# Performance work log

Measured on AMD Instinct MI355X. Metric: run time of the kernel, lower is better.

## Reference

```python
import jax, jax.numpy as jnp
from jax import lax
import numpy as np

D = 1024      # input_size
H = D // 2    # proj hidden
T = 25        # num_ner_labels
B, S = 64, 512


def setup_inputs() -> dict:
    key = jax.random.key(0)
    ks = jax.random.split(key, 8)
    sc1 = 1.0 / np.sqrt(D)
    sc2 = 1.0 / np.sqrt(H)
    return {
        "encoder_out": jax.random.normal(ks[0], (B, S, D), dtype=jnp.float32),
        "W1": jax.random.uniform(ks[1], (D, H), jnp.float32, -sc1, sc1),
        "b1": jax.random.uniform(ks[2], (H,), jnp.float32, -sc1, sc1),
        "W2": jax.random.uniform(ks[3], (H, T), jnp.float32, -sc2, sc2),
        "b2": jax.random.uniform(ks[4], (T,), jnp.float32, -sc2, sc2),
        "start_trans": jax.random.uniform(ks[5], (T,), jnp.float32, -0.1, 0.1),
        "end_trans": jax.random.uniform(ks[6], (T,), jnp.float32, -0.1, 0.1),
        "trans": jax.random.uniform(ks[7], (T, T), jnp.float32, -0.1, 0.1),
        "ner_labels": jax.random.randint(jax.random.fold_in(key, 1), (B, S), 0, T, dtype=jnp.int64),
        "mask": jnp.ones((B, S), dtype=bool),
    }


def _crf_nll(emissions, start_trans, end_trans, trans, labels, mask):
    # torchcrf negative mean log-likelihood, batch_first
    maskf = mask.astype(emissions.dtype)
    # numerator: score of gold path
    em_at_tag = jnp.take_along_axis(emissions, labels[..., None], axis=2)[..., 0]  # [B,S]
    score0 = start_trans[labels[:, 0]] + em_at_tag[:, 0]
    trans_sc = trans[labels[:, :-1], labels[:, 1:]]                                # [B,S-1]
    step_score = (trans_sc + em_at_tag[:, 1:]) * maskf[:, 1:]
    last_idx = mask.sum(axis=1).astype(jnp.int32) - 1
    last_tag = jnp.take_along_axis(labels, last_idx[:, None].astype(labels.dtype), axis=1)[:, 0]
    numerator = score0 + step_score.sum(axis=1) + end_trans[last_tag]
    # denominator: log partition via forward algorithm (scan over time)
    alpha0 = start_trans[None, :] + emissions[:, 0]                                # [B,T]
    em_rest = jnp.swapaxes(emissions[:, 1:], 0, 1)                                 # [S-1,B,T]
    m_rest = jnp.swapaxes(mask[:, 1:], 0, 1)                                       # [S-1,B]

    def step(alpha, xs):
        em_t, m_t = xs
        new = jax.scipy.special.logsumexp(
            alpha[:, :, None] + trans[None, :, :] + em_t[:, None, :], axis=1)
        return jnp.where(m_t[:, None], new, alpha), None

    alpha, _ = lax.scan(step, alpha0, (em_rest, m_rest))
    log_Z = jax.scipy.special.logsumexp(alpha + end_trans[None, :], axis=1)        # [B]
    return -jnp.mean(numerator - log_Z)


def reference(encoder_out, W1, b1, W2, b2, start_trans, end_trans, trans, ner_labels, mask):
    h = jax.nn.gelu(encoder_out @ W1 + b1, approximate=False)  # dropout is eval-mode identity
    emissions = h @ W2 + b2                                    # [B,S,T]
    return _crf_nll(emissions, start_trans, end_trans, trans, ner_labels, mask)
```

## Files before the change

kernel.cpp:

```cpp
#include <hip/hip_runtime.h>
#include <math.h>

#define DD 1024
#define HH 512
#define TT 25
#define BB 64
#define SS 512
#define MM (BB*SS)
#define NC 32

typedef __attribute__((ext_vector_type(8))) short short8;
typedef __attribute__((ext_vector_type(4))) float floatx4;
typedef __attribute__((ext_vector_type(16))) float floatx16;

static __device__ __forceinline__ unsigned short f2bf(float f) {
  unsigned u = __float_as_uint(f);
  u = (u + 0x7FFFu + ((u >> 16) & 1u)) >> 16;
  return (unsigned short)u;
}
static __device__ __forceinline__ float bf2f(unsigned short s) {
  return __uint_as_float(((unsigned)s) << 16);
}
static __device__ __forceinline__ float rl(float v, int i) {
  return __int_as_float(__builtin_amdgcn_readlane(__float_as_int(v), i));
}
static __device__ __forceinline__ void load_lds16(const void* g, void* l) {
  __builtin_amdgcn_global_load_lds(
      (const __attribute__((address_space(1))) unsigned int*)g,
      (__attribute__((address_space(3))) unsigned int*)l, 16, 0, 0);
}
union U4S8 { uint4 u; short8 s; };

__global__ __launch_bounds__(256) void k_prep(
    const float* __restrict__ W1, const float* __restrict__ W2,
    unsigned short* __restrict__ W1T2, unsigned short* __restrict__ W2p) {
  const int t = threadIdx.x;
  if (blockIdx.y < 8) {
    __shared__ unsigned short tile[64 * 72];
    const int k0 = blockIdx.x * 64, n0 = blockIdx.y * 64;
    #pragma unroll
    for (int it = 0; it < 16; it++) {
      int idx = t + it * 256;
      int kk = idx >> 6, nn = idx & 63;
      tile[nn * 72 + kk] = f2bf(W1[(size_t)(k0 + kk) * HH + n0 + nn]);
    }
    __syncthreads();
    #pragma unroll
    for (int it = 0; it < 4; it++) {
      int idx = (t + it * 256) * 4;
      int nn = idx >> 6, kk = idx & 63;
      ushort4 v;
      v.x = tile[nn * 72 + kk];     v.y = tile[nn * 72 + kk + 1];
      v.z = tile[nn * 72 + kk + 2]; v.w = tile[nn * 72 + kk + 3];
      int kt = (k0 >> 5) + (kk >> 5), kkk = kk & 31;
      *(ushort4*)(W1T2 + (size_t)kt * (HH * 32) + (n0 + nn) * 32 + kkk) = v;
    }
  } else {
    #pragma unroll
    for (int e = 0; e < 4; e++) {
      int idx = blockIdx.x * 1024 + t + e * 256;
      int row = idx >> 9, k = idx & 511;
      float v = (row < TT) ? W2[(size_t)k * TT + row] : 0.f;
      W2p[(size_t)row * HH + k] = f2bf(v);
    }
  }
}

__global__ __launch_bounds__(256, 3) void k_emis(
    const float* __restrict__ X, const unsigned short* __restrict__ W1T2,
    const float* __restrict__ b1, const unsigned short* __restrict__ W2p,
    const float* __restrict__ b2, float* __restrict__ em) {
  __shared__ __attribute__((aligned(16))) short lds[20480];

  const int tid  = threadIdx.x;
  const int lane = tid & 63;
  const int w    = tid >> 6;
  const int l15  = lane & 15;
  const int kc   = lane >> 4;
  const int m0   = blockIdx.x * 64;
  const int colbase = blockIdx.y * 256;

  floatx4 acc[4][4];
  #pragma unroll
  for (int a = 0; a < 4; a++)
    #pragma unroll
    for (int b = 0; b < 4; b++)
      acc[a][b] = (floatx4){0.f, 0.f, 0.f, 0.f};

  const int am = tid >> 2;
  const int ac = tid & 3;
  const float* Xrow = X + (size_t)(m0 + am) * DD + ac * 8;

  const unsigned short* gW = W1T2 + (size_t)(colbase + w * 64) * 32 + lane * 8;

  {
    float4 xv0 = *(const float4*)(Xrow);
    float4 xv1 = *(const float4*)(Xrow + 4);
    unsigned p0 = (unsigned)f2bf(xv0.x) | ((unsigned)f2bf(xv0.y) << 16);
    unsigned p1 = (unsigned)f2bf(xv0.z) | ((unsigned)f2bf(xv0.w) << 16);
    unsigned p2 = (unsigned)f2bf(xv1.x) | ((unsigned)f2bf(xv1.y) << 16);
    unsigned p3 = (unsigned)f2bf(xv1.z) | ((unsigned)f2bf(xv1.w) << 16);
    *(uint4*)(lds + am * 32 + ac * 8) = make_uint4(p0, p1, p2, p3);
  }
  {
    short* lW = lds + 4096 + w * 2048;
    #pragma unroll
    for (int j = 0; j < 4; j++)
      load_lds16(gW + j * 512, lW + j * 512);
  }
  float4 yv0 = *(const float4*)(Xrow + 32);
  float4 yv1 = *(const float4*)(Xrow + 36);
  __syncthreads();

  for (int t = 0; t < 32; ++t) {
    const int cur = t & 1, nxt = cur ^ 1;
    short* sXc = lds + cur * 2048;
    short* sBc = lds + 4096 + cur * 8192;

    float4 zv0, zv1;
    if (t < 31) {
      const unsigned short* g = gW + (size_t)(t + 1) * (HH * 32);
      short* lW = lds + 4096 + nxt * 8192 + w * 2048;
      #pragma unroll
      for (int j = 0; j < 4; j++)
        load_lds16(g + j * 512, lW + j * 512);
      if (t < 30) {
        zv0 = *(const float4*)(Xrow + (t + 2) * 32);
        zv1 = *(const float4*)(Xrow + (t + 2) * 32 + 4);
      }
    }

    short8 af[4], bfr[4];
    #pragma unroll
    for (int mt = 0; mt < 4; mt++)
      af[mt] = *(const short8*)(sXc + (mt * 16 + l15) * 32 + kc * 8);
    #pragma unroll
    for (int nt = 0; nt < 4; nt++)
      bfr[nt] = *(const short8*)(sBc + (w * 64 + nt * 16 + l15) * 32 + kc * 8);
    #pragma unroll
    for (int mt = 0; mt < 4; mt++)
      #pragma unroll
      for (int nt = 0; nt < 4; nt++)
        acc[mt][nt] = __builtin_amdgcn_mfma_f32_16x16x32_bf16(af[mt], bfr[nt], acc[mt][nt], 0, 0, 0);

    if (t < 31) {
      unsigned p0 = (unsigned)f2bf(yv0.x) | ((unsigned)f2bf(yv0.y) << 16);
      unsigned p1 = (unsigned)f2bf(yv0.z) | ((unsigned)f2bf(yv0.w) << 16);
      unsigned p2 = (unsigned)f2bf(yv1.x) | ((unsigned)f2bf(yv1.y) << 16);
      unsigned p3 = (unsigned)f2bf(yv1.z) | ((unsigned)f2bf(yv1.w) << 16);
      *(uint4*)(lds + nxt * 2048 + am * 32 + ac * 8) = make_uint4(p0, p1, p2, p3);
      if (t < 30) { yv0 = zv0; yv1 = zv1; }
    }
    __syncthreads();
  }

  short* sH = lds;
  float* sC = (float*)(lds + 8448);
  const int mt_g = w & 1, kh_g = w >> 1;

  short8 w2f[2][4];
  #pragma unroll
  for (int nt2 = 0; nt2 < 2; nt2++)
    #pragma unroll
    for (int ks = 0; ks < 4; ks++)
      w2f[nt2][ks] = *(const short8*)(W2p + (size_t)(nt2 * 16 + l15) * HH
                                      + colbase + kh_g * 128 + ks * 32 + kc * 8);

  #pragma unroll
  for (int half = 0; half < 2; half++) {
    __syncthreads();
    #pragma unroll
    for (int mt2 = 0; mt2 < 2; mt2++) {
      int mt = half * 2 + mt2;
      #pragma unroll
      for (int nt = 0; nt < 4; nt++) {
        int n = w * 64 + nt * 16 + l15;
        float bias = b1[colbase + n];
        #pragma unroll
        for (int r = 0; r < 4; r++) {
          int ml = mt2 * 16 + kc * 4 + r;
          float v = acc[mt][nt][r] + bias;
          float g = 0.5f * v * (1.0f + erff(v * 0.70710678118654752f));
          sH[ml * 264 + n] = (short)f2bf(g);
        }
      }
    }
    __syncthreads();
    #pragma unroll
    for (int nt2 = 0; nt2 < 2; nt2++) {
      floatx4 c2 = (floatx4){0.f, 0.f, 0.f, 0.f};
      #pragma unroll
      for (int ks = 0; ks < 4; ks++) {
        short8 a2 = *(const short8*)(sH + (mt_g * 16 + l15) * 264 + kh_g * 128 + ks * 32 + kc * 8);
        c2 = __builtin_amdgcn_mfma_f32_16x16x32_bf16(a2, w2f[nt2][ks], c2, 0, 0, 0);
      }
      #pragma unroll
      for (int r = 0; r < 4; r++)
        sC[kh_g * 1024 + (mt_g * 16 + kc * 4 + r) * 32 + nt2 * 16 + l15] = c2[r];
    }
    __syncthreads();
    for (int o = tid; o < 32 * TT; o += 256) {
      int m = o / TT, t = o % TT;
      float val = sC[m * 32 + t] + sC[1024 + m * 32 + t];
      if (blockIdx.y == 0) val += b2[t];
      atomicAdd(em + (size_t)(m0 + half * 32 + m) * TT + t, val);
    }
  }
}

__global__ __launch_bounds__(64) void k_chunk(
    const float* __restrict__ em, const float* __restrict__ trans,
    float* __restrict__ Mats) {
  const int b = blockIdx.x, c = blockIdx.y;
  const int lane = threadIdx.x;
  const int h = lane >> 5;
  const int n = lane & 31;
  const float* emb = em + (size_t)b * SS * TT;

  unsigned a1p[4], a2p[4];
  #pragma unroll
  for (int p = 0; p < 4; p++) {
    int i0 = h * 8 + 2 * p, i1 = i0 + 1;
    unsigned lo = (n < TT && i0 < TT) ? (unsigned)f2bf(__expf(trans[i0 * TT + n])) : 0u;
    unsigned hi = (n < TT && i1 < TT) ? (unsigned)f2bf(__expf(trans[i1 * TT + n])) : 0u;
    a1p[p] = lo | (hi << 16);
    int j0 = 16 + h * 8 + 2 * p, j1 = j0 + 1;
    lo = (n < TT && j0 < TT) ? (unsigned)f2bf(__expf(trans[j0 * TT + n])) : 0u;
    hi = (n < TT && j1 < TT) ? (unsigned)f2bf(__expf(trans[j1 * TT + n])) : 0u;
    a2p[p] = lo | (hi << 16);
  }
  U4S8 A1, A2;
  A1.u = make_uint4(a1p[0], a1p[1], a1p[2], a1p[3]);
  A2.u = make_uint4(a2p[0], a2p[1], a2p[2], a2p[3]);

  unsigned bp1[4], bp2[4];
  #pragma unroll
  for (int p = 0; p < 4; p++) {
    int k0 = h * 8 + 2 * p;
    bp1[p] = ((k0 == n) ? 0x3F80u : 0u) | ((k0 + 1 == n) ? 0x3F800000u : 0u);
    int k2 = 16 + h * 8 + 2 * p;
    bp2[p] = ((k2 == n) ? 0x3F80u : 0u) | ((k2 + 1 == n) ? 0x3F800000u : 0u);
  }

  const int s0 = 1 + c * 16;
  const int nst = (s0 + 16 <= SS) ? 16 : (SS - s0);

  float emv[16], f[16];
  #pragma unroll
  for (int e = 0; e < 16; e++) {
    int r = (e & 3) + 8 * (e >> 2) + 4 * h;
    emv[e] = (r < TT) ? emb[s0 * TT + r] : 0.f;
  }

  for (int t = 0; t < nst; t++) {
    const float rs = (t == 8) ? 32.0f : 0.0f;
    float ex[16];
    #pragma unroll
    for (int e = 0; e < 16; e++) ex[e] = __expf(emv[e] - rs);
    int sn = (s0 + t + 1 < SS) ? s0 + t + 1 : SS - 1;
    #pragma unroll
    for (int e = 0; e < 16; e++) {
      int r = (e & 3) + 8 * (e >> 2) + 4 * h;
      emv[e] = (r < TT) ? emb[sn * TT + r] : 0.f;
    }
    U4S8 B1, B2;
    B1.u = make_uint4(bp1[0], bp1[1], bp1[2], bp1[3]);
    B2.u = make_uint4(bp2[0], bp2[1], bp2[2], bp2[3]);
    floatx16 D = __builtin_amdgcn_mfma_f32_32x32x16_bf16(A1.s, B1.s,
                   __builtin_amdgcn_mfma_f32_32x32x16_bf16(A2.s, B2.s,
                     (floatx16){0.f,0.f,0.f,0.f,0.f,0.f,0.f,0.f,
                                0.f,0.f,0.f,0.f,0.f,0.f,0.f,0.f}, 0,0,0), 0,0,0);
    #pragma unroll
    for (int e = 0; e < 16; e++) f[e] = D[e] * ex[e];
    if (t == nst - 1) break;
    unsigned P[16];
    #pragma unroll
    for (int p = 0; p < 8; p++)
      P[p] = (unsigned)f2bf(f[2 * p]) | ((unsigned)f2bf(f[2 * p + 1]) << 16);
    unsigned sp[8];
    #pragma unroll
    for (int p = 0; p < 8; p++)
      sp[p] = (unsigned)__shfl_xor((int)P[p], 32);
    bool up = (h == 1);
    bp1[0] = up ? sp[2] : P[0];
    bp1[1] = up ? sp[3] : P[1];
    bp1[2] = up ? P[2] : sp[0];
    bp1[3] = up ? P[3] : sp[1];
    bp2[0] = up ? sp[6] : P[4];
    bp2[1] = up ? sp[7] : P[5];
    bp2[2] = up ? P[6] : sp[4];
    bp2[3] = up ? P[7] : sp[5];
  }

  if (n < TT) {
    float* Mc = Mats + ((size_t)(b * NC + c)) * (TT * TT) + n * TT;
    #pragma unroll
    for (int e = 0; e < 16; e++) {
      int r = (e & 3) + 8 * (e >> 2) + 4 * h;
      if (r < TT) Mc[r] = __logf(f[e]) + 32.0f;
    }
  }
}

__global__ __launch_bounds__(64) void k_comb(
    const float* __restrict__ em, const float* __restrict__ start,
    const float* __restrict__ endt, const float* __restrict__ trans,
    const int* __restrict__ labels, const float* __restrict__ Mats,
    float* __restrict__ partial) {
  const int b = blockIdx.x;
  const int tid = threadIdx.x;
  const float* emb = em + (size_t)b * SS * TT;
  const int* lab = labels + b * SS;

  float part = 0.f;
  for (int s = tid; s < SS; s += 64) {
    int l = lab[s];
    if (s == 0) part += start[l] + emb[l];
    else        part += trans[lab[s - 1] * TT + l] + emb[s * TT + l];
  }
  #pragma unroll
  for (int off = 32; off; off >>= 1) part += __shfl_xor(part, off);
  float num = part + endt[lab[SS - 1]];

  const int jj = (tid < TT) ? tid : 0;
  float a = (tid < TT) ? start[tid] + emb[tid] : -1e30f;
  const float* Mb = Mats + (size_t)b * NC * (TT * TT);
  for (int c = 0; c < NC; c++) {
    const float* Mc = Mb + c * (TT * TT);
    float col[TT];
    float mxc = -1e30f;
    #pragma unroll
    for (int i = 0; i < TT; i++) {
      col[i] = Mc[i * TT + jj];
      mxc = fmaxf(mxc, col[i]);
    }
    float a0 = __builtin_amdgcn_readfirstlane(a);
    float p = __expf(a - a0);
    float d0 = 0.f, d1 = 0.f, d2 = 0.f, d3 = 0.f;
    #pragma unroll
    for (int i = 0; i < 24; i += 4) {
      d0 = fmaf(rl(p, i + 0), __expf(col[i + 0] - mxc), d0);
      d1 = fmaf(rl(p, i + 1), __expf(col[i + 1] - mxc), d1);
      d2 = fmaf(rl(p, i + 2), __expf(col[i + 2] - mxc), d2);
      d3 = fmaf(rl(p, i + 3), __expf(col[i + 3] - mxc), d3);
    }
    d0 = fmaf(rl(p, 24), __expf(col[24] - mxc), d0);
    float anew = a0 + mxc + __logf((d0 + d1) + (d2 + d3));
    a = (tid < TT) ? anew : -1e30f;
  }

  float v = (tid < TT) ? a + endt[tid] : -1e30f;
  float mx = v;
  #pragma unroll
  for (int off = 16; off; off >>= 1) mx = fmaxf(mx, __shfl_xor(mx, off, 32));
  float e = (tid < TT) ? __expf(v - mx) : 0.f;
  #pragma unroll
  for (int off = 16; off; off >>= 1) e += __shfl_xor(e, off, 32);
  if (tid == 0) partial[b] = (mx + __logf(e)) - num;
}

__global__ void k_final(const float* __restrict__ partial, float* __restrict__ out) {
  int tid = threadIdx.x;
  float v = partial[tid];
  #pragma unroll
  for (int off = 32; off; off >>= 1) v += __shfl_xor(v, off);
  if (tid == 0) out[0] = v * (1.0f / 64.0f);
}

extern "C" void kernel_launch(void* const* d_in, const int* in_sizes, int n_in,
                              void* d_out, int out_size, void* d_ws, size_t ws_size,
                              hipStream_t stream) {
  const float* X   = (const float*)d_in[0];
  const float* W1  = (const float*)d_in[1];
  const float* b1  = (const float*)d_in[2];
  const float* W2  = (const float*)d_in[3];
  const float* b2  = (const float*)d_in[4];
  const float* st  = (const float*)d_in[5];
  const float* en  = (const float*)d_in[6];
  const float* tr  = (const float*)d_in[7];
  const int* labels = (const int*)d_in[8];

  char* ws = (char*)d_ws;
  unsigned short* W1T2 = (unsigned short*)ws;
  unsigned short* W2p  = (unsigned short*)(ws + 0x100000);
  float* em            = (float*)(ws + 0x110000);
  float* Mats          = (float*)(ws + 0x430000);
  float* partial       = (float*)(ws + 0x930000);

  k_prep <<<dim3(16, 9), 256, 0, stream>>>(W1, W2, W1T2, W2p);
  hipMemsetAsync(em, 0, (size_t)MM * TT * sizeof(float), stream);
  k_emis <<<dim3(512, 2), 256, 0, stream>>>(X, W1T2, b1, W2p, b2, em);
  k_chunk<<<dim3(BB, NC), 64, 0, stream>>>(em, tr, Mats);
  k_comb <<<BB, 64, 0, stream>>>(em, st, en, tr, labels, Mats, partial);
  k_final<<<1, 64, 0, stream>>>(partial, (float*)d_out);
}
```

Baseline: 335.2 us.

## Single-buffer X tile in LDS and raise occupancy to four blocks per CU

Drops the double-buffered bf16 X tile in LDS in favor of one buffer, shrinking shared memory so launch bounds can ask for four blocks per CU instead of three. The loop is restructured into convert-store X, barrier with hand-written vmcnt/lgkmcnt waits, read fragments, MFMA, then a second barrier. W1 tiles keep async double buffering. The aim is more resident waves to hide latency. The cost is two barriers per K step and exposed X conversion, and the fixed vmcnt(6) count relies on the exact number of outstanding loads.

```diff
diff --git a/kernel.cpp b/kernel.cpp
--- a/kernel.cpp
+++ b/kernel.cpp
@@ -66,11 +66,11 @@
   }
 }
 
-__global__ __launch_bounds__(256, 3) void k_emis(
+__global__ __launch_bounds__(256, 4) void k_emis(
     const float* __restrict__ X, const unsigned short* __restrict__ W1T2,
     const float* __restrict__ b1, const unsigned short* __restrict__ W2p,
     const float* __restrict__ b2, float* __restrict__ em) {
-  __shared__ __attribute__((aligned(16))) short lds[20480];
+  __shared__ __attribute__((aligned(16))) short lds[18432];
 
   const int tid  = threadIdx.x;
   const int lane = tid & 63;
@@ -94,64 +94,59 @@
   const unsigned short* gW = W1T2 + (size_t)(colbase + w * 64) * 32 + lane * 8;
 
   {
-    float4 xv0 = *(const float4*)(Xrow);
-    float4 xv1 = *(const float4*)(Xrow + 4);
-    unsigned p0 = (unsigned)f2bf(xv0.x) | ((unsigned)f2bf(xv0.y) << 16);
-    unsigned p1 = (unsigned)f2bf(xv0.z) | ((unsigned)f2bf(xv0.w) << 16);
-    unsigned p2 = (unsigned)f2bf(xv1.x) | ((unsigned)f2bf(xv1.y) << 16);
-    unsigned p3 = (unsigned)f2bf(xv1.z) | ((unsigned)f2bf(xv1.w) << 16);
-    *(uint4*)(lds + am * 32 + ac * 8) = make_uint4(p0, p1, p2, p3);
-  }
-  {
-    short* lW = lds + 4096 + w * 2048;
+    short* lW = lds + 2048 + w * 2048;
     #pragma unroll
     for (int j = 0; j < 4; j++)
       load_lds16(gW + j * 512, lW + j * 512);
   }
-  float4 yv0 = *(const float4*)(Xrow + 32);
-  float4 yv1 = *(const float4*)(Xrow + 36);
-  __syncthreads();
+  float4 yv0 = *(const float4*)(Xrow);
+  float4 yv1 = *(const float4*)(Xrow + 4);
 
   for (int t = 0; t < 32; ++t) {
-    const int cur = t & 1, nxt = cur ^ 1;
-    short* sXc = lds + cur * 2048;
-    short* sBc = lds + 4096 + cur * 8192;
+    short* sBc = lds + 2048 + (t & 1) * 8192;
 
     float4 zv0, zv1;
     if (t < 31) {
+      short* lW = lds + 2048 + ((t + 1) & 1) * 8192 + w * 2048;
       const unsigned short* g = gW + (size_t)(t + 1) * (HH * 32);
-      short* lW = lds + 4096 + nxt * 8192 + w * 2048;
       #pragma unroll
       for (int j = 0; j < 4; j++)
         load_lds16(g + j * 512, lW + j * 512);
-      if (t < 30) {
-        zv0 = *(const float4*)(Xrow + (t + 2) * 32);
-        zv1 = *(const float4*)(Xrow + (t + 2) * 32 + 4);
-      }
-    }
-
-    short8 af[4], bfr[4];
-    #pragma unroll
-    for (int mt = 0; mt < 4; mt++)
-      af[mt] = *(const short8*)(sXc + (mt * 16 + l15) * 32 + kc * 8);
-    #pragma unroll
-    for (int nt = 0; nt < 4; nt++)
-      bfr[nt] = *(const short8*)(sBc + (w * 64 + nt * 16 + l15) * 32 + kc * 8);
-    #pragma unroll
-    for (int mt = 0; mt < 4; mt++)
-      #pragma unroll
-      for (int nt = 0; nt < 4; nt++)
-        acc[mt][nt] = __builtin_amdgcn_mfma_f32_16x16x32_bf16(af[mt], bfr[nt], acc[mt][nt], 0, 0, 0);
-
-    if (t < 31) {
+      zv0 = *(const float4*)(Xrow + (t + 1) * 32);
+      zv1 = *(const float4*)(Xrow + (t + 1) * 32 + 4);
+    }
+
+    {
       unsigned p0 = (unsigned)f2bf(yv0.x) | ((unsigned)f2bf(yv0.y) << 16);
       unsigned p1 = (unsigned)f2bf(yv0.z) | ((unsigned)f2bf(yv0.w) << 16);
       unsigned p2 = (unsigned)f2bf(yv1.x) | ((unsigned)f2bf(yv1.y) << 16);
       unsigned p3 = (unsigned)f2bf(yv1.z) | ((unsigned)f2bf(yv1.w) << 16);
-      *(uint4*)(lds + nxt * 2048 + am * 32 + ac * 8) = make_uint4(p0, p1, p2, p3);
-      if (t < 30) { yv0 = zv0; yv1 = zv1; }
-    }
-    __syncthreads();
+      *(uint4*)(lds + am * 32 + ac * 8) = make_uint4(p0, p1, p2, p3);
+    }
+    if (t < 31) { yv0 = zv0; yv1 = zv1; }
+
+    asm volatile("s_waitcnt vmcnt(6) lgkmcnt(0)" ::: "memory");
+    __builtin_amdgcn_s_barrier();
+    asm volatile("" ::: "memory");
+
+    short8 af[4], bfr[4];
+    #pragma unroll
+    for (int mt = 0; mt < 4; mt++)
+      af[mt] = *(const short8*)(lds + (mt * 16 + l15) * 32 + kc * 8);
+    #pragma unroll
+    for (int nt = 0; nt < 4; nt++)
+      bfr[nt] = *(const short8*)(sBc + (w * 64 + nt * 16 + l15) * 32 + kc * 8);
+    asm volatile("s_waitcnt lgkmcnt(0)" ::: "memory");
+    __builtin_amdgcn_sched_barrier(0);
+    #pragma unroll
+    for (int mt = 0; mt < 4; mt++)
+      #pragma unroll
+      for (int nt = 0; nt < 4; nt++)
+        acc[mt][nt] = __builtin_amdgcn_mfma_f32_16x16x32_bf16(af[mt], bfr[nt], acc[mt][nt], 0, 0, 0);
+
+    asm volatile("" ::: "memory");
+    __builtin_amdgcn_s_barrier();
+    asm volatile("" ::: "memory");
   }
 
   short* sH = lds;
```

Measured after the change: 303.3 us. 1.11x faster.
